# Optimization experiments

Hardware: AMD Instinct MI355X
Metric: run time of the kernel (lower is better)

## Reference

```python
import jax, jax.numpy as jnp
import numpy as np
import math

DIM = 2048
N_HEADS = 32
N_KV_HEADS = 8
HEAD_DIM = DIM // N_HEADS  # 64
N_REP = N_HEADS // N_KV_HEADS  # 4
BSZ, SEQ = 2, 2048


def setup_inputs() -> dict:
    key = jax.random.key(0)
    ks = jax.random.split(key, 8)
    x = jax.random.normal(ks[0], (BSZ, SEQ, DIM), dtype=jnp.float32)
    # rotary tables, [seq, head_dim//2]
    inv_freq = 1.0 / (10000.0 ** (np.arange(0, HEAD_DIM, 2, dtype=np.float32) / HEAD_DIM))
    t = np.arange(SEQ, dtype=np.float32)
    freqs = np.outer(t, inv_freq)
    freqs_cos = jnp.asarray(np.cos(freqs))
    freqs_sin = jnp.asarray(np.sin(freqs))
    s = 0.02
    wq = jax.random.normal(ks[1], (DIM, N_HEADS * HEAD_DIM), dtype=jnp.float32) * s
    wk = jax.random.normal(ks[2], (DIM, N_KV_HEADS * HEAD_DIM), dtype=jnp.float32) * s
    wv = jax.random.normal(ks[3], (DIM, N_KV_HEADS * HEAD_DIM), dtype=jnp.float32) * s
    wo = jax.random.normal(ks[4], (N_HEADS * HEAD_DIM, DIM), dtype=jnp.float32) * s
    return {"x": x, "freqs_cos": freqs_cos, "freqs_sin": freqs_sin,
            "wq": wq, "wk": wk, "wv": wv, "wo": wo}


def _apply_rotary(xq, xk, cos, sin):
    # xq: [b,s,h,d], xk: [b,s,kh,d]; cos/sin: [s, d//2]
    def rot(t):
        tr = t[..., 0::2]  # even -> real
        ti = t[..., 1::2]  # odd  -> imag
        c = cos[None, :, None, :]
        s_ = sin[None, :, None, :]
        or_ = tr * c - ti * s_
        oi_ = tr * s_ + ti * c
        # interleave back: [..., d//2, 2] -> [..., d]
        return jnp.stack([or_, oi_], axis=-1).reshape(t.shape)
    return rot(xq), rot(xk)


def reference(x, freqs_cos, freqs_sin, wq, wk, wv, wo):
    b, s, _ = x.shape
    xq = (x @ wq).reshape(b, s, N_HEADS, HEAD_DIM)
    xk = (x @ wk).reshape(b, s, N_KV_HEADS, HEAD_DIM)
    xv = (x @ wv).reshape(b, s, N_KV_HEADS, HEAD_DIM)
    xq, xk = _apply_rotary(xq, xk, freqs_cos, freqs_sin)
    # repeat_kv: [b,s,kh,d] -> [b,s,kh*n_rep,d]
    xk = jnp.repeat(xk, N_REP, axis=2)
    xv = jnp.repeat(xv, N_REP, axis=2)
    # [b,h,s,d]
    q = xq.transpose(0, 2, 1, 3)
    k = xk.transpose(0, 2, 1, 3)
    v = xv.transpose(0, 2, 1, 3)
    scale = 1.0 / math.sqrt(HEAD_DIM)
    scores = jnp.einsum('bhqd,bhkd->bhqk', q, k) * scale
    causal = jnp.tril(jnp.ones((s, s), dtype=bool))
    scores = jnp.where(causal[None, None], scores, jnp.float32(-jnp.inf))
    probs = jax.nn.softmax(scores, axis=-1)
    out = jnp.einsum('bhqk,bhkd->bhqd', probs, v)  # [b,h,s,d]
    out = out.transpose(0, 2, 1, 3).reshape(b, s, N_HEADS * HEAD_DIM)
    return out @ wo
```

## Files before the change

kernel.cpp:

```cpp
#include <hip/hip_runtime.h>
#include <hip/hip_bf16.h>

typedef __attribute__((ext_vector_type(8))) short short8;
typedef __attribute__((ext_vector_type(4))) float f32x4;

__device__ __forceinline__ unsigned short f2bf(float f) {
  union { float f; unsigned u; } v; v.f = f;
  unsigned r = v.u + 0x7FFFu + ((v.u >> 16) & 1u);
  return (unsigned short)(r >> 16);
}
__device__ __forceinline__ float bf2f(unsigned short h) {
  union { unsigned u; float f; } v; v.u = ((unsigned)h) << 16;
  return v.f;
}
__device__ __forceinline__ unsigned pkbf(float a, float b) {
  __hip_bfloat162 h = __float22bfloat162_rn(float2{a, b});
  union { __hip_bfloat162 h; unsigned u; } cv; cv.h = h;
  return cv.u;
}

__global__ void cast_f32_bf16(const float* __restrict__ in, unsigned short* __restrict__ out, int n4) {
  int i = blockIdx.x * blockDim.x + threadIdx.x;
  if (i >= n4) return;
  float4 v = ((const float4*)in)[i];
  ushort4 o;
  o.x = f2bf(v.x); o.y = f2bf(v.y); o.z = f2bf(v.z); o.w = f2bf(v.w);
  ((ushort4*)out)[i] = o;
}

__global__ void transpose_cast_all(const float* __restrict__ wq, const float* __restrict__ wk,
                                   const float* __restrict__ wv, const float* __restrict__ wo,
                                   unsigned short* __restrict__ wt, unsigned short* __restrict__ wot) {
  __shared__ float tile[32][33];
  const int z = blockIdx.z;
  const float* src;
  unsigned short* dst;
  int N;
  if (z == 0) { src = wq; dst = wt; N = 2048; }
  else if (z == 1) { src = wk; dst = wt + 2048ull * 2048; N = 512; }
  else if (z == 2) { src = wv; dst = wt + 2560ull * 2048; N = 512; }
  else { src = wo; dst = wot; N = 2048; }
  const int K = 2048;
  int n0 = blockIdx.x * 32, k0 = blockIdx.y * 32;
  if (n0 >= N) return;
  int x = threadIdx.x, y = threadIdx.y;
#pragma unroll
  for (int j = 0; j < 4; ++j) tile[y + 8 * j][x] = src[(size_t)(k0 + y + 8 * j) * N + n0 + x];
  __syncthreads();
#pragma unroll
  for (int j = 0; j < 4; ++j) dst[(size_t)(n0 + y + 8 * j) * K + k0 + x] = f2bf(tile[x][y + 8 * j]);
}

__global__ void v_transpose(const unsigned short* __restrict__ qkv, unsigned short* __restrict__ vt) {
  __shared__ unsigned short tile[32][33];
  int c0 = blockIdx.x * 32, r0 = blockIdx.y * 32;
  int x = threadIdx.x, y = threadIdx.y;
#pragma unroll
  for (int j = 0; j < 4; ++j)
    tile[y + 8 * j][x] = qkv[(size_t)(r0 + y + 8 * j) * 3072 + 2560 + c0 + x];
  __syncthreads();
  int b = r0 >> 11;
  int kvh = c0 >> 6;
#pragma unroll
  for (int j = 0; j < 4; ++j) {
    int c = c0 + y + 8 * j, r = r0 + x;
    vt[((size_t)(b * 8 + kvh) * 64 + (c & 63)) * 2048 + (r & 2047)] = tile[x][y + 8 * j];
  }
}

template <int OUT_BF16>
__global__ __launch_bounds__(256, 2) void gemm_bt(const unsigned short* __restrict__ A,
                                                  const unsigned short* __restrict__ Bt,
                                                  void* __restrict__ Cv, int K, int ldc) {
  __shared__ alignas(16) unsigned short As[128 * 32];
  __shared__ alignas(16) unsigned short Bs[128 * 32];
  const int t = threadIdx.x;
  const int lane = t & 63, w = t >> 6;
  const int l15 = lane & 15, quad = lane >> 4;
  const int bn0 = blockIdx.x * 128, bm0 = blockIdx.y * 128;
  const int wm = (w >> 1) * 64, wn = (w & 1) * 64;
  const unsigned short* Ab = A + (size_t)bm0 * K;
  const unsigned short* Bb = Bt + (size_t)bn0 * K;

  f32x4 acc[4][4];
  const f32x4 zf = {0.f, 0.f, 0.f, 0.f};
#pragma unroll
  for (int i = 0; i < 4; ++i)
#pragma unroll
    for (int j = 0; j < 4; ++j) acc[i][j] = zf;

  for (int k0 = 0; k0 < K; k0 += 32) {
    __syncthreads();
#pragma unroll
    for (int r = 0; r < 2; ++r) {
      int e = r * 256 + t;
      const unsigned short* ga = Ab + (size_t)(e >> 2) * K + k0 + (e & 3) * 8;
      __builtin_amdgcn_global_load_lds((const __attribute__((address_space(1))) void*)ga,
                                       (__attribute__((address_space(3))) void*)(As + e * 8), 16, 0, 0);
      const unsigned short* gb = Bb + (size_t)(e >> 2) * K + k0 + (e & 3) * 8;
      __builtin_amdgcn_global_load_lds((const __attribute__((address_space(1))) void*)gb,
                                       (__attribute__((address_space(3))) void*)(Bs + e * 8), 16, 0, 0);
    }
    __syncthreads();
    short8 af[4], bf[4];
#pragma unroll
    for (int i = 0; i < 4; ++i)
      af[i] = *reinterpret_cast<const short8*>(As + (wm + i * 16 + l15) * 32 + quad * 8);
#pragma unroll
    for (int j = 0; j < 4; ++j)
      bf[j] = *reinterpret_cast<const short8*>(Bs + (wn + j * 16 + l15) * 32 + quad * 8);
#pragma unroll
    for (int i = 0; i < 4; ++i)
#pragma unroll
      for (int j = 0; j < 4; ++j)
        acc[i][j] = __builtin_amdgcn_mfma_f32_16x16x32_bf16(af[i], bf[j], acc[i][j], 0, 0, 0);
  }
#pragma unroll
  for (int i = 0; i < 4; ++i)
#pragma unroll
    for (int j = 0; j < 4; ++j)
#pragma unroll
      for (int r = 0; r < 4; ++r) {
        size_t row = (size_t)(bm0 + wm + i * 16 + quad * 4 + r);
        size_t col = (size_t)(bn0 + wn + j * 16 + l15);
        if (OUT_BF16)
          ((unsigned short*)Cv)[row * ldc + col] = f2bf(acc[i][j][r]);
        else
          ((float*)Cv)[row * ldc + col] = acc[i][j][r];
      }
}

__global__ void rope_k(unsigned short* __restrict__ qkv, const float* __restrict__ fcos,
                       const float* __restrict__ fsin) {
  int tid = blockIdx.x * 256 + threadIdx.x;
  int row = tid >> 8, p = tid & 255;
  int col = 2048 + 2 * p;
  int s = row & 2047;
  int fi = p & 31;
  float c = fcos[s * 32 + fi], sn = fsin[s * 32 + fi];
  unsigned int* ptr = (unsigned int*)(qkv + (size_t)row * 3072 + col);
  unsigned int pr = *ptr;
  float xr = bf2f((unsigned short)(pr & 0xFFFFu));
  float xi = bf2f((unsigned short)(pr >> 16));
  float orr = xr * c - xi * sn;
  float oi = xr * sn + xi * c;
  *ptr = ((unsigned)f2bf(oi) << 16) | (unsigned)f2bf(orr);
}

__global__ __launch_bounds__(256, 4) void flash_attn(const unsigned short* __restrict__ qkv,
                                                     const unsigned short* __restrict__ vt,
                                                     const float* __restrict__ fcos,
                                                     const float* __restrict__ fsin,
                                                     unsigned short* __restrict__ out) {
  __shared__ alignas(16) unsigned short Ks[64 * 64];
  __shared__ alignas(16) unsigned short Vs[64 * 64];
  __shared__ alignas(16) unsigned short Ps[128 * 64];
  __shared__ float Ls[128];
  const int t = threadIdx.x, lane = t & 63, w = t >> 6;
  const int l15 = lane & 15, quad = lane >> 4;
  const int h = blockIdx.y, b = blockIdx.z;
  const int qb = ((int)blockIdx.x ^ (15 * (h >> 4))) & 15;
  const int q0 = qb * 128;
  const int kvh = h >> 2;
  const size_t rowB = (size_t)b * 2048;
  const unsigned short* Qg = qkv + (rowB + q0) * 3072 + h * 64;
  const unsigned short* Kg = qkv + rowB * 3072 + 2048 + kvh * 64;
  const unsigned short* Vtg = vt + (size_t)(b * 8 + kvh) * 64 * 2048;
  const float SC = 0.18033688011112042f;

  short8 qf[2][2];
#pragma unroll
  for (int mt = 0; mt < 2; ++mt)
#pragma unroll
    for (int s = 0; s < 2; ++s) {
      int qrow = w * 32 + mt * 16 + l15;
      short8 raw = *reinterpret_cast<const short8*>(Qg + (size_t)qrow * 3072 + s * 32 + quad * 8);
      f32x4 c4 = *reinterpret_cast<const f32x4*>(fcos + (size_t)(q0 + qrow) * 32 + s * 16 + quad * 4);
      f32x4 s4 = *reinterpret_cast<const f32x4*>(fsin + (size_t)(q0 + qrow) * 32 + s * 16 + quad * 4);
      short8 o;
#pragma unroll
      for (int k = 0; k < 4; ++k) {
        float xr = bf2f((unsigned short)raw[2 * k]);
        float xi = bf2f((unsigned short)raw[2 * k + 1]);
        o[2 * k] = (short)f2bf((xr * c4[k] - xi * s4[k]) * SC);
        o[2 * k + 1] = (short)f2bf((xr * s4[k] + xi * c4[k]) * SC);
      }
      qf[mt][s] = o;
    }

  const f32x4 zf = {0.f, 0.f, 0.f, 0.f};
  f32x4 oacc[2][4];
#pragma unroll
  for (int mt = 0; mt < 2; ++mt)
#pragma unroll
    for (int nt = 0; nt < 4; ++nt) oacc[mt][nt] = zf;
  float lsum[2] = {0.f, 0.f};

  const int kb_end = 2 * qb + 2;
  const int srow = t >> 3, sc8 = t & 7;
  const int soff = srow * 64 + ((sc8 ^ (srow & 7)) * 8);
  const int asw = l15 & 7;
  short8 kreg[2], vreg[2];
#pragma unroll
  for (int r = 0; r < 2; ++r) {
    kreg[r] = *reinterpret_cast<const short8*>(Kg + (size_t)(srow + 32 * r) * 3072 + sc8 * 8);
    vreg[r] = *reinterpret_cast<const short8*>(Vtg + (size_t)(srow + 32 * r) * 2048 + sc8 * 8);
  }

  for (int kb = 0; kb < kb_end; ++kb) {
    __syncthreads();
#pragma unroll
    for (int r = 0; r < 2; ++r) {
      *reinterpret_cast<short8*>(Ks + soff + r * 32 * 64) = kreg[r];
      *reinterpret_cast<short8*>(Vs + soff + r * 32 * 64) = vreg[r];
    }
    __syncthreads();
    if (kb + 1 < kb_end) {
#pragma unroll
      for (int r = 0; r < 2; ++r) {
        kreg[r] = *reinterpret_cast<const short8*>(Kg + (size_t)((kb + 1) * 64 + srow + 32 * r) * 3072 + sc8 * 8);
        vreg[r] = *reinterpret_cast<const short8*>(Vtg + (size_t)(srow + 32 * r) * 2048 + (kb + 1) * 64 + sc8 * 8);
      }
    }
    const int qmaxw = q0 + w * 32 + 31;
    if (kb * 64 > qmaxw) continue;
    const bool needMask = (kb * 64 + 63) > (q0 + w * 32);

#pragma unroll
    for (int kvt = 0; kvt < 4; ++kvt) {
      f32x4 st0 = zf, st1 = zf;
#pragma unroll
      for (int s = 0; s < 2; ++s) {
        short8 kf = *reinterpret_cast<const short8*>(Ks + (kvt * 16 + l15) * 64 + ((s * 4 + quad) ^ asw) * 8);
        st0 = __builtin_amdgcn_mfma_f32_16x16x32_bf16(kf, qf[0][s], st0, 0, 0, 0);
        st1 = __builtin_amdgcn_mfma_f32_16x16x32_bf16(kf, qf[1][s], st1, 0, 0, 0);
      }
      const int pcol = ((kvt * 2 + (quad >> 1)) ^ asw) * 8 + (quad & 1) * 4;
      if (needMask) {
        const int kvb = kb * 64 + kvt * 16 + quad * 4;
#pragma unroll
        for (int qt = 0; qt < 2; ++qt) {
          const f32x4 stv = qt ? st1 : st0;
          const int qg = q0 + w * 32 + qt * 16 + l15;
          float p[4];
#pragma unroll
          for (int r = 0; r < 4; ++r) {
            float pv = __builtin_amdgcn_exp2f(stv[r]);
            p[r] = (kvb + r > qg) ? 0.f : pv;
          }
          lsum[qt] += (p[0] + p[1]) + (p[2] + p[3]);
          *reinterpret_cast<uint2*>(Ps + (size_t)(w * 32 + qt * 16 + l15) * 64 + pcol) =
              make_uint2(pkbf(p[0], p[1]), pkbf(p[2], p[3]));
        }
      } else {
#pragma unroll
        for (int qt = 0; qt < 2; ++qt) {
          const f32x4 stv = qt ? st1 : st0;
          float p[4];
#pragma unroll
          for (int r = 0; r < 4; ++r) p[r] = __builtin_amdgcn_exp2f(stv[r]);
          lsum[qt] += (p[0] + p[1]) + (p[2] + p[3]);
          *reinterpret_cast<uint2*>(Ps + (size_t)(w * 32 + qt * 16 + l15) * 64 + pcol) =
              make_uint2(pkbf(p[0], p[1]), pkbf(p[2], p[3]));
        }
      }
    }

#pragma unroll
    for (int s = 0; s < 2; ++s) {
      short8 vf[4];
#pragma unroll
      for (int nt = 0; nt < 4; ++nt)
        vf[nt] = *reinterpret_cast<const short8*>(Vs + (nt * 16 + l15) * 64 + ((s * 4 + quad) ^ asw) * 8);
#pragma unroll
      for (int mt = 0; mt < 2; ++mt) {
        short8 pf = *reinterpret_cast<const short8*>(Ps + (size_t)(w * 32 + mt * 16 + l15) * 64 + ((s * 4 + quad) ^ asw) * 8);
#pragma unroll
        for (int nt = 0; nt < 4; ++nt)
          oacc[mt][nt] = __builtin_amdgcn_mfma_f32_16x16x32_bf16(pf, vf[nt], oacc[mt][nt], 0, 0, 0);
      }
    }
  }

#pragma unroll
  for (int qt = 0; qt < 2; ++qt) {
    lsum[qt] += __shfl_xor(lsum[qt], 16, 64);
    lsum[qt] += __shfl_xor(lsum[qt], 32, 64);
  }
  if (quad == 0) {
    Ls[w * 32 + l15] = lsum[0];
    Ls[w * 32 + 16 + l15] = lsum[1];
  }
  float linv[2][4];
#pragma unroll
  for (int mt = 0; mt < 2; ++mt)
#pragma unroll
    for (int r = 0; r < 4; ++r) linv[mt][r] = 1.f / Ls[w * 32 + mt * 16 + quad * 4 + r];

#pragma unroll
  for (int mt = 0; mt < 2; ++mt)
#pragma unroll
    for (int nt = 0; nt < 4; ++nt)
#pragma unroll
      for (int r = 0; r < 4; ++r) {
        size_t row = rowB + (size_t)(q0 + w * 32 + mt * 16 + quad * 4 + r);
        size_t col = (size_t)h * 64 + nt * 16 + l15;
        out[row * 2048 + col] = f2bf(oacc[mt][nt][r] * linv[mt][r]);
      }
}

extern "C" void kernel_launch(void* const* d_in, const int* in_sizes, int n_in, void* d_out,
                              int out_size, void* d_ws, size_t ws_size, hipStream_t stream) {
  const float* x = (const float*)d_in[0];
  const float* fcos = (const float*)d_in[1];
  const float* fsin = (const float*)d_in[2];
  const float* wq = (const float*)d_in[3];
  const float* wk = (const float*)d_in[4];
  const float* wv = (const float*)d_in[5];
  const float* wo = (const float*)d_in[6];

  char* ws = (char*)d_ws;
  unsigned short* xb = (unsigned short*)ws;
  unsigned short* wt = (unsigned short*)(ws + 16777216ull);
  unsigned short* wot = (unsigned short*)(ws + 29360128ull);
  unsigned short* qkv = (unsigned short*)(ws + 37748736ull);
  unsigned short* attno = (unsigned short*)(ws + 62914560ull);
  unsigned short* vt = xb;

  cast_f32_bf16<<<8192, 256, 0, stream>>>(x, xb, 2097152);
  transpose_cast_all<<<dim3(64, 64, 4), dim3(32, 8), 0, stream>>>(wq, wk, wv, wo, wt, wot);

  gemm_bt<1><<<dim3(24, 32), 256, 0, stream>>>(xb, wt, qkv, 2048, 3072);
  rope_k<<<4096, 256, 0, stream>>>(qkv, fcos, fsin);
  v_transpose<<<dim3(16, 128), dim3(32, 8), 0, stream>>>(qkv, vt);
  flash_attn<<<dim3(16, 32, 2), 256, 0, stream>>>(qkv, vt, fcos, fsin, attno);
  gemm_bt<0><<<dim3(16, 32), 256, 0, stream>>>(attno, wot, d_out, 2048, 2048);
}
```

Measured before the change: 297.9 us.

## Fuse prep kernels, widen GEMM K-tile with swizzle, write V transposed from GEMM

Merges the x cast and weight transpose-casts into one prep launch. The QKV GEMM's V-column tiles now write V directly in transposed layout, which removes the separate v_transpose kernel and shrinks the qkv row stride to 2560. The GEMM K-step doubles to 64 with an XOR-swizzled LDS layout to reduce bank conflicts and halve loop/barrier overhead, at the cost of twice the LDS per block, which may limit occupancy. The transposed V stores are strided 8-byte writes, which may be less coalesced.

```diff
diff --git a/kernel.cpp b/kernel.cpp
--- a/kernel.cpp
+++ b/kernel.cpp
@@ -19,61 +19,49 @@
   return cv.u;
 }
 
-__global__ void cast_f32_bf16(const float* __restrict__ in, unsigned short* __restrict__ out, int n4) {
-  int i = blockIdx.x * blockDim.x + threadIdx.x;
-  if (i >= n4) return;
-  float4 v = ((const float4*)in)[i];
-  ushort4 o;
-  o.x = f2bf(v.x); o.y = f2bf(v.y); o.z = f2bf(v.z); o.w = f2bf(v.w);
-  ((ushort4*)out)[i] = o;
-}
-
-__global__ void transpose_cast_all(const float* __restrict__ wq, const float* __restrict__ wk,
-                                   const float* __restrict__ wv, const float* __restrict__ wo,
-                                   unsigned short* __restrict__ wt, unsigned short* __restrict__ wot) {
+__global__ void prep(const float* __restrict__ x, const float* __restrict__ wq,
+                     const float* __restrict__ wk, const float* __restrict__ wv,
+                     const float* __restrict__ wo, unsigned short* __restrict__ xb,
+                     unsigned short* __restrict__ wt, unsigned short* __restrict__ wot) {
+  const int z = blockIdx.z, tid = threadIdx.x;
+  if (z == 0) {
+    int id = blockIdx.y * 64 + blockIdx.x;
+#pragma unroll
+    for (int rep = 0; rep < 2; ++rep) {
+      int i = (rep * 4096 + id) * 256 + tid;
+      float4 v = ((const float4*)x)[i];
+      ushort4 o;
+      o.x = f2bf(v.x); o.y = f2bf(v.y); o.z = f2bf(v.z); o.w = f2bf(v.w);
+      ((ushort4*)xb)[i] = o;
+    }
+    return;
+  }
   __shared__ float tile[32][33];
-  const int z = blockIdx.z;
   const float* src;
   unsigned short* dst;
   int N;
-  if (z == 0) { src = wq; dst = wt; N = 2048; }
-  else if (z == 1) { src = wk; dst = wt + 2048ull * 2048; N = 512; }
-  else if (z == 2) { src = wv; dst = wt + 2560ull * 2048; N = 512; }
+  if (z == 1) { src = wq; dst = wt; N = 2048; }
+  else if (z == 2) { src = wk; dst = wt + 2048ull * 2048; N = 512; }
+  else if (z == 3) { src = wv; dst = wt + 2560ull * 2048; N = 512; }
   else { src = wo; dst = wot; N = 2048; }
   const int K = 2048;
   int n0 = blockIdx.x * 32, k0 = blockIdx.y * 32;
   if (n0 >= N) return;
-  int x = threadIdx.x, y = threadIdx.y;
-#pragma unroll
-  for (int j = 0; j < 4; ++j) tile[y + 8 * j][x] = src[(size_t)(k0 + y + 8 * j) * N + n0 + x];
+  int xx = tid & 31, yy = tid >> 5;
+#pragma unroll
+  for (int j = 0; j < 4; ++j) tile[yy + 8 * j][xx] = src[(size_t)(k0 + yy + 8 * j) * N + n0 + xx];
   __syncthreads();
 #pragma unroll
-  for (int j = 0; j < 4; ++j) dst[(size_t)(n0 + y + 8 * j) * K + k0 + x] = f2bf(tile[x][y + 8 * j]);
-}
-
-__global__ void v_transpose(const unsigned short* __restrict__ qkv, unsigned short* __restrict__ vt) {
-  __shared__ unsigned short tile[32][33];
-  int c0 = blockIdx.x * 32, r0 = blockIdx.y * 32;
-  int x = threadIdx.x, y = threadIdx.y;
-#pragma unroll
-  for (int j = 0; j < 4; ++j)
-    tile[y + 8 * j][x] = qkv[(size_t)(r0 + y + 8 * j) * 3072 + 2560 + c0 + x];
-  __syncthreads();
-  int b = r0 >> 11;
-  int kvh = c0 >> 6;
-#pragma unroll
-  for (int j = 0; j < 4; ++j) {
-    int c = c0 + y + 8 * j, r = r0 + x;
-    vt[((size_t)(b * 8 + kvh) * 64 + (c & 63)) * 2048 + (r & 2047)] = tile[x][y + 8 * j];
-  }
-}
-
-template <int OUT_BF16>
-__global__ __launch_bounds__(256, 2) void gemm_bt(const unsigned short* __restrict__ A,
-                                                  const unsigned short* __restrict__ Bt,
-                                                  void* __restrict__ Cv, int K, int ldc) {
-  __shared__ alignas(16) unsigned short As[128 * 32];
-  __shared__ alignas(16) unsigned short Bs[128 * 32];
+  for (int j = 0; j < 4; ++j) dst[(size_t)(n0 + yy + 8 * j) * K + k0 + xx] = f2bf(tile[xx][yy + 8 * j]);
+}
+
+template <int MODE>
+__global__ __launch_bounds__(256, 2) void gemm_bt64(const unsigned short* __restrict__ A,
+                                                    const unsigned short* __restrict__ Bt,
+                                                    void* __restrict__ Cv, int K, int ldc,
+                                                    unsigned short* __restrict__ vt) {
+  __shared__ alignas(16) unsigned short As[128 * 64];
+  __shared__ alignas(16) unsigned short Bs[128 * 64];
   const int t = threadIdx.x;
   const int lane = t & 63, w = t >> 6;
   const int l15 = lane & 15, quad = lane >> 4;
@@ -81,6 +69,7 @@
   const int wm = (w >> 1) * 64, wn = (w & 1) * 64;
   const unsigned short* Ab = A + (size_t)bm0 * K;
   const unsigned short* Bb = Bt + (size_t)bn0 * K;
+  const int asw = l15 & 7;
 
   f32x4 acc[4][4];
   const f32x4 zf = {0.f, 0.f, 0.f, 0.f};
@@ -89,45 +78,66 @@
 #pragma unroll
     for (int j = 0; j < 4; ++j) acc[i][j] = zf;
 
-  for (int k0 = 0; k0 < K; k0 += 32) {
+  for (int k0 = 0; k0 < K; k0 += 64) {
     __syncthreads();
 #pragma unroll
-    for (int r = 0; r < 2; ++r) {
+    for (int r = 0; r < 4; ++r) {
       int e = r * 256 + t;
-      const unsigned short* ga = Ab + (size_t)(e >> 2) * K + k0 + (e & 3) * 8;
+      int row = e >> 3, cslot = e & 7;
+      int cg = cslot ^ (row & 7);
+      const unsigned short* ga = Ab + (size_t)row * K + k0 + cg * 8;
       __builtin_amdgcn_global_load_lds((const __attribute__((address_space(1))) void*)ga,
                                        (__attribute__((address_space(3))) void*)(As + e * 8), 16, 0, 0);
-      const unsigned short* gb = Bb + (size_t)(e >> 2) * K + k0 + (e & 3) * 8;
+      const unsigned short* gb = Bb + (size_t)row * K + k0 + cg * 8;
       __builtin_amdgcn_global_load_lds((const __attribute__((address_space(1))) void*)gb,
                                        (__attribute__((address_space(3))) void*)(Bs + e * 8), 16, 0, 0);
     }
     __syncthreads();
-    short8 af[4], bf[4];
+#pragma unroll
+    for (int s = 0; s < 2; ++s) {
+      short8 af[4], bf[4];
+#pragma unroll
+      for (int i = 0; i < 4; ++i)
+        af[i] = *reinterpret_cast<const short8*>(As + (wm + i * 16 + l15) * 64 + (((s * 4 + quad) ^ asw) * 8));
+#pragma unroll
+      for (int j = 0; j < 4; ++j)
+        bf[j] = *reinterpret_cast<const short8*>(Bs + (wn + j * 16 + l15) * 64 + (((s * 4 + quad) ^ asw) * 8));
+#pragma unroll
+      for (int i = 0; i < 4; ++i)
+#pragma unroll
+        for (int j = 0; j < 4; ++j)
+          acc[i][j] = __builtin_amdgcn_mfma_f32_16x16x32_bf16(af[i], bf[j], acc[i][j], 0, 0, 0);
+    }
+  }
+
+  if (MODE == 1 && bn0 >= 2560) {
+    const int b = bm0 >> 11;
+#pragma unroll
+    for (int i = 0; i < 4; ++i) {
+      int srow = (bm0 + wm + i * 16 + quad * 4) & 2047;
+#pragma unroll
+      for (int j = 0; j < 4; ++j) {
+        int vcol = bn0 - 2560 + wn + j * 16 + l15;
+        int kvh = vcol >> 6, d = vcol & 63;
+        uint2 pk = make_uint2(pkbf(acc[i][j][0], acc[i][j][1]), pkbf(acc[i][j][2], acc[i][j][3]));
+        *reinterpret_cast<uint2*>(vt + ((size_t)(b * 8 + kvh) * 64 + d) * 2048 + srow) = pk;
+      }
+    }
+  } else {
 #pragma unroll
     for (int i = 0; i < 4; ++i)
-      af[i] = *reinterpret_cast<const short8*>(As + (wm + i * 16 + l15) * 32 + quad * 8);
-#pragma unroll
-    for (int j = 0; j < 4; ++j)
-      bf[j] = *reinterpret_cast<const short8*>(Bs + (wn + j * 16 + l15) * 32 + quad * 8);
-#pragma unroll
-    for (int i = 0; i < 4; ++i)
 #pragma unroll
       for (int j = 0; j < 4; ++j)
-        acc[i][j] = __builtin_amdgcn_mfma_f32_16x16x32_bf16(af[i], bf[j], acc[i][j], 0, 0, 0);
-  }
-#pragma unroll
-  for (int i = 0; i < 4; ++i)
-#pragma unroll
-    for (int j = 0; j < 4; ++j)
-#pragma unroll
-      for (int r = 0; r < 4; ++r) {
-        size_t row = (size_t)(bm0 + wm + i * 16 + quad * 4 + r);
-        size_t col = (size_t)(bn0 + wn + j * 16 + l15);
-        if (OUT_BF16)
-          ((unsigned short*)Cv)[row * ldc + col] = f2bf(acc[i][j][r]);
-        else
-          ((float*)Cv)[row * ldc + col] = acc[i][j][r];
-      }
+#pragma unroll
+        for (int r = 0; r < 4; ++r) {
+          size_t row = (size_t)(bm0 + wm + i * 16 + quad * 4 + r);
+          size_t col = (size_t)(bn0 + wn + j * 16 + l15);
+          if (MODE == 1)
+            ((unsigned short*)Cv)[row * ldc + col] = f2bf(acc[i][j][r]);
+          else
+            ((float*)Cv)[row * ldc + col] = acc[i][j][r];
+        }
+  }
 }
 
 __global__ void rope_k(unsigned short* __restrict__ qkv, const float* __restrict__ fcos,
@@ -138,7 +148,7 @@
   int s = row & 2047;
   int fi = p & 31;
   float c = fcos[s * 32 + fi], sn = fsin[s * 32 + fi];
-  unsigned int* ptr = (unsigned int*)(qkv + (size_t)row * 3072 + col);
+  unsigned int* ptr = (unsigned int*)(qkv + (size_t)row * 2560 + col);
   unsigned int pr = *ptr;
   float xr = bf2f((unsigned short)(pr & 0xFFFFu));
   float xi = bf2f((unsigned short)(pr >> 16));
@@ -163,8 +173,8 @@
   const int q0 = qb * 128;
   const int kvh = h >> 2;
   const size_t rowB = (size_t)b * 2048;
-  const unsigned short* Qg = qkv + (rowB + q0) * 3072 + h * 64;
-  const unsigned short* Kg = qkv + rowB * 3072 + 2048 + kvh * 64;
+  const unsigned short* Qg = qkv + (rowB + q0) * 2560 + h * 64;
+  const unsigned short* Kg = qkv + rowB * 2560 + 2048 + kvh * 64;
   const unsigned short* Vtg = vt + (size_t)(b * 8 + kvh) * 64 * 2048;
   const float SC = 0.18033688011112042f;
 
@@ -174,7 +184,7 @@
 #pragma unroll
     for (int s = 0; s < 2; ++s) {
       int qrow = w * 32 + mt * 16 + l15;
-      short8 raw = *reinterpret_cast<const short8*>(Qg + (size_t)qrow * 3072 + s * 32 + quad * 8);
+      short8 raw = *reinterpret_cast<const short8*>(Qg + (size_t)qrow * 2560 + s * 32 + quad * 8);
       f32x4 c4 = *reinterpret_cast<const f32x4*>(fcos + (size_t)(q0 + qrow) * 32 + s * 16 + quad * 4);
       f32x4 s4 = *reinterpret_cast<const f32x4*>(fsin + (size_t)(q0 + qrow) * 32 + s * 16 + quad * 4);
       short8 o;
@@ -203,7 +213,7 @@
   short8 kreg[2], vreg[2];
 #pragma unroll
   for (int r = 0; r < 2; ++r) {
-    kreg[r] = *reinterpret_cast<const short8*>(Kg + (size_t)(srow + 32 * r) * 3072 + sc8 * 8);
+    kreg[r] = *reinterpret_cast<const short8*>(Kg + (size_t)(srow + 32 * r) * 2560 + sc8 * 8);
     vreg[r] = *reinterpret_cast<const short8*>(Vtg + (size_t)(srow + 32 * r) * 2048 + sc8 * 8);
   }
 
@@ -218,7 +228,7 @@
     if (kb + 1 < kb_end) {
 #pragma unroll
       for (int r = 0; r < 2; ++r) {
-        kreg[r] = *reinterpret_cast<const short8*>(Kg + (size_t)((kb + 1) * 64 + srow + 32 * r) * 3072 + sc8 * 8);
+        kreg[r] = *reinterpret_cast<const short8*>(Kg + (size_t)((kb + 1) * 64 + srow + 32 * r) * 2560 + sc8 * 8);
         vreg[r] = *reinterpret_cast<const short8*>(Vtg + (size_t)(srow + 32 * r) * 2048 + (kb + 1) * 64 + sc8 * 8);
       }
     }
@@ -324,15 +334,12 @@
   unsigned short* wt = (unsigned short*)(ws + 16777216ull);
   unsigned short* wot = (unsigned short*)(ws + 29360128ull);
   unsigned short* qkv = (unsigned short*)(ws + 37748736ull);
-  unsigned short* attno = (unsigned short*)(ws + 62914560ull);
-  unsigned short* vt = xb;
-
-  cast_f32_bf16<<<8192, 256, 0, stream>>>(x, xb, 2097152);
-  transpose_cast_all<<<dim3(64, 64, 4), dim3(32, 8), 0, stream>>>(wq, wk, wv, wo, wt, wot);
-
-  gemm_bt<1><<<dim3(24, 32), 256, 0, stream>>>(xb, wt, qkv, 2048, 3072);
+  unsigned short* attno = (unsigned short*)(ws + 58720256ull);
+  unsigned short* vt = (unsigned short*)(ws + 75497472ull);
+
+  prep<<<dim3(64, 64, 5), 256, 0, stream>>>(x, wq, wk, wv, wo, xb, wt, wot);
+  gemm_bt64<1><<<dim3(24, 32), 256, 0, stream>>>(xb, wt, qkv, 2048, 2560, vt);
   rope_k<<<4096, 256, 0, stream>>>(qkv, fcos, fsin);
-  v_transpose<<<dim3(16, 128), dim3(32, 8), 0, stream>>>(qkv, vt);
   flash_attn<<<dim3(16, 32, 2), 256, 0, stream>>>(qkv, vt, fcos, fsin, attno);
-  gemm_bt<0><<<dim3(16, 32), 256, 0, stream>>>(attno, wot, d_out, 2048, 2048);
-}
+  gemm_bt64<0><<<dim3(16, 32), 256, 0, stream>>>(attno, wot, d_out, 2048, 2048, nullptr);
+}
```

After: 272.0 us. 1.1x faster.
